# Optimization experiments

Hardware: AMD Instinct MI355X
Metric: run time of the kernel (lower is better)

Reference implementation:

```python
import jax, jax.numpy as jnp
import numpy as np

SCORE_THR = 0.3
NMS_IOU = 0.3
TOPK = 100          # fixed candidate budget replacing dynamic boolean masking
IMAGE_SHAPE = (512, 512)  # (H, W); letterbox_image=False so scale is direct


def pool_nms(heat):
    # 3x3 max-pool peak-NMS: keep only local maxima
    pooled = jax.lax.reduce_window(heat, -jnp.inf, jax.lax.max,
                                   (1, 1, 3, 3), (1, 1, 1, 1), 'SAME')
    return heat * (pooled == heat).astype(heat.dtype)


def setup_inputs() -> dict:
    key = jax.random.key(0)
    k1, k2, k3 = jax.random.split(key, 3)
    hm = jax.random.uniform(k1, (32, 80, 128, 128), dtype=jnp.float32)
    wh = jax.random.uniform(k2, (32, 2, 128, 128), dtype=jnp.float32) * 8.0
    offset = jax.random.uniform(k3, (32, 2, 128, 128), dtype=jnp.float32)
    return {"hm": hm, "wh": wh, "offset": offset}


def reference(hm, wh, offset):
    B, C, H, W = hm.shape
    HW = H * W
    heat = pool_nms(hm)
    heat = heat.transpose(0, 2, 3, 1).reshape(B, HW, C)       # [B,HW,C]
    whf = wh.transpose(0, 2, 3, 1).reshape(B, HW, 2)           # [B,HW,2]
    off = offset.transpose(0, 2, 3, 1).reshape(B, HW, 2)       # [B,HW,2]

    conf = heat.max(-1)                                        # [B,HW]
    cls = jnp.argmax(heat, -1)                                 # [B,HW]

    idx = jnp.arange(HW)
    xv = (idx % W).astype(hm.dtype)
    yv = (idx // W).astype(hm.dtype)
    cx = xv[None, :] + off[..., 0]
    cy = yv[None, :] + off[..., 1]
    bw = whf[..., 0]
    bh = whf[..., 1]
    # normalized xyxy boxes, as in decode_bbox
    boxes = jnp.stack([(cx - bw / 2) / W, (cy - bh / 2) / H,
                       (cx + bw / 2) / W, (cy + bh / 2) / H], -1)  # [B,HW,4]

    scores = jnp.where(conf > SCORE_THR, conf, 0.0)
    top_s, top_i = jax.lax.top_k(scores, TOPK)                 # sorted desc
    tb = jnp.take_along_axis(boxes, top_i[..., None], axis=1)  # [B,K,4]
    tc = jnp.take_along_axis(cls, top_i, axis=1)               # [B,K]
    valid = top_s > SCORE_THR                                  # [B,K]

    # per-class greedy NMS on score-sorted candidates (fixed size K)
    area = (tb[..., 2] - tb[..., 0]) * (tb[..., 3] - tb[..., 1])
    lt = jnp.maximum(tb[:, :, None, :2], tb[:, None, :, :2])
    rb = jnp.minimum(tb[:, :, None, 2:], tb[:, None, :, 2:])
    whi = jnp.clip(rb - lt, 0.0)
    inter = whi[..., 0] * whi[..., 1]
    iou = inter / (area[:, :, None] + area[:, None, :] - inter + 1e-9)
    supmat = (iou > NMS_IOU) & (tc[:, :, None] == tc[:, None, :])  # [B,K,K]

    j = jnp.arange(TOPK)

    def body(i, keep):
        alive_i = jnp.take(keep, i, axis=1)[:, None]           # [B,1]
        sup = jnp.take(supmat, i, axis=1) & (j[None, :] > i) & alive_i
        return keep & ~sup

    keep = jax.lax.fori_loop(0, TOPK, body, valid)             # [B,K]

    # centernet_correct_boxes with letterbox_image=False: scale to image size
    ih, iw = IMAGE_SHAPE
    cxy = (tb[..., :2] + tb[..., 2:]) / 2
    cwh = tb[..., 2:] - tb[..., :2]
    mins = cxy - cwh / 2
    maxs = cxy + cwh / 2
    scale = jnp.array([iw, ih, iw, ih], hm.dtype)
    bimg = jnp.concatenate([mins, maxs], -1) * scale           # [B,K,4]

    dets = jnp.concatenate([bimg, top_s[..., None],
                            tc[..., None].astype(hm.dtype)], -1)  # [B,K,6]
    return jnp.where(keep[..., None], dets, 0.0)
```

## Files before the change

kernel.cpp:

```cpp
#include <hip/hip_runtime.h>
#include <hip/hip_bf16.h>
#include <stdint.h>

#define HH 128
#define WW 128
#define CC 80
#define HW (HH * WW)
#define BB 32
#define TOPK 100
#define TROWS 8
#define NTHREADS 256
#define SCORE_THR 0.3f
#define NMS_IOU 0.3f
#define BUF 512
#define MINT 0x3E99999Bu

__device__ __forceinline__ void async_load16(const float* gp, const float* lp) {
    auto g = (const __attribute__((address_space(1))) void*)(uintptr_t)gp;
    auto l = (__attribute__((address_space(3))) void*)(uint32_t)(uintptr_t)lp;
    __builtin_amdgcn_global_load_lds(g, l, 16, 0, 0);
}

template <int G>
__global__ __launch_bounds__(NTHREADS, 8)
void heat_reduce(const float* __restrict__ hm,
                 float* __restrict__ conf_out,
                 unsigned char* __restrict__ cls_out) {
    constexpr int CPG = CC / G;
    const int g      = blockIdx.x % G;
    const int stripe = (blockIdx.x / G) & 15;
    const int b      = blockIdx.x / (16 * G);
    const int y0     = stripe * TROWS;
    const int tid    = threadIdx.x;
    const int lane   = tid & 63;
    const int wv     = tid >> 6;
    const int x      = tid & 127;
    const int h      = tid >> 7;
    const int c0     = g * CPG;

    __shared__ float tileS[2][(TROWS + 2) * WW];

    auto load = [&](int c, int buf) {
        const float* base = hm + (size_t)(b * CC + c) * HW;
        for (int chunk = wv; chunk < 5; chunk += 4) {
            int e    = chunk * 64 + lane;
            int row  = e >> 5;
            int col  = (e & 31) << 2;
            int y    = y0 - 1 + row;
            y = min(max(y, 0), HH - 1);
            async_load16(base + (size_t)y * WW + col,
                         &tileS[buf][chunk * 256]);
        }
    };

    float conf[4] = {0.f, 0.f, 0.f, 0.f};
    int   cls[4]  = {c0, c0, c0, c0};

    const int xl = (x > 0) ? x - 1 : x;
    const int xr = (x < WW - 1) ? x + 1 : x;

    load(c0, 0);
    __syncthreads();

    for (int cc = 0; cc < CPG; ++cc) {
        const int c  = c0 + cc;
        const int bb = cc & 1;
        if (cc + 1 < CPG) load(c + 1, bb ^ 1);

        float rmax[6], center[6];
#pragma unroll
        for (int k = 0; k < 6; ++k) {
            const float* row = &tileS[bb][(h * 4 + k) * WW];
            float l = row[xl], m = row[x], r = row[xr];
            center[k] = m;
            rmax[k]   = fmaxf(fmaxf(l, m), r);
        }
#pragma unroll
        for (int r = 0; r < 4; ++r) {
            float val  = center[r + 1];
            float pool = fmaxf(fmaxf(rmax[r], rmax[r + 1]), rmax[r + 2]);
            float heat = (val == pool) ? val : 0.0f;
            if (heat > conf[r]) { conf[r] = heat; cls[r] = c; }
        }
        __syncthreads();
    }

#pragma unroll
    for (int r = 0; r < 4; ++r) {
        int y = y0 + h * 4 + r;
        size_t idx = (size_t)b * HW + (size_t)y * WW + x;
        conf_out[idx * G + g] = conf[r];
        cls_out[idx * G + g]  = (unsigned char)cls[r];
    }
}

template <int G>
__global__ __launch_bounds__(NTHREADS, 1)
void select_nms(const float* __restrict__ conf_part,
                const unsigned char* __restrict__ cls_part,
                const float* __restrict__ wh,
                const float* __restrict__ offset,
                float* __restrict__ out) {
    const int b    = blockIdx.x;
    const int tid  = threadIdx.x;
    const int lane = tid & 63;
    const int wid  = tid >> 6;
    constexpr int VALS = HW / NTHREADS;

    __shared__ int wsum[4];
    __shared__ unsigned int sCnt;
    __shared__ unsigned long long keys[BUF];

    unsigned u[VALS];
#pragma unroll
    for (int k = 0; k < VALS; ++k) {
        int i = k * NTHREADS + tid;
        float best;
        if constexpr (G == 4) {
            float4 cf = *(const float4*)&conf_part[(size_t)(b * HW + i) * 4];
            best = cf.x;
            if (cf.y > best) best = cf.y;
            if (cf.z > best) best = cf.z;
            if (cf.w > best) best = cf.w;
        } else {
            best = conf_part[(size_t)b * HW + i];
        }
        u[k] = (best > SCORE_THR) ? __float_as_uint(best) : 0u;
    }

    auto blockCount = [&](unsigned T) -> int {
        int c = 0;
#pragma unroll
        for (int k = 0; k < VALS; ++k) c += (u[k] >= T);
        for (int o = 32; o > 0; o >>= 1) c += __shfl_down(c, o, 64);
        if (lane == 0) wsum[wid] = c;
        __syncthreads();
        int tot = wsum[0] + wsum[1] + wsum[2] + wsum[3];
        __syncthreads();
        return tot;
    };

    unsigned V;
    {
        unsigned lo = MINT, hi = 0x3F800001u;
        int cl = blockCount(lo);
        if (cl < TOPK) {
            V = lo;
        } else {
            while (hi - lo > 1u) {
                unsigned mid = lo + ((hi - lo) >> 1);
                if (blockCount(mid) >= TOPK) lo = mid; else hi = mid;
            }
            V = lo;
        }
    }

    if (tid == 0) sCnt = 0;
    for (int i = tid; i < BUF; i += NTHREADS) keys[i] = 0ull;
    __syncthreads();
#pragma unroll
    for (int k = 0; k < VALS; ++k) {
        if (u[k] >= V) {
            int i = k * NTHREADS + tid;
            unsigned pos = atomicAdd(&sCnt, 1u);
            if (pos < BUF)
                keys[pos] = ((unsigned long long)u[k] << 32) |
                            (unsigned)(HW - 1 - i);
        }
    }
    __syncthreads();
    int cnt = (int)sCnt;
    if (cnt > BUF) cnt = BUF;

    int n = 1;
    while (n < cnt) n <<= 1;
    for (int k = 2; k <= n; k <<= 1) {
        for (int j = k >> 1; j > 0; j >>= 1) {
            for (int i = tid; i < n; i += NTHREADS) {
                int p = i ^ j;
                if (p > i) {
                    unsigned long long a = keys[i], bb2 = keys[p];
                    bool asc_seg = ((i & k) != 0);
                    bool sw = asc_seg ? (a > bb2) : (a < bb2);
                    if (sw) { keys[i] = bb2; keys[p] = a; }
                }
            }
            __syncthreads();
        }
    }

    __shared__ float bx[TOPK][4];
    __shared__ float barea[TOPK];
    __shared__ float bsc[TOPK];
    __shared__ int   bcls[TOPK];
    __shared__ int   keep[TOPK];

    if (tid < TOPK) {
        unsigned long long kk = keys[tid];
        float sc = __uint_as_float((unsigned)(kk >> 32));
        int   i  = HW - 1 - (int)(kk & 0xFFFFFFFFull);
        int   y  = (i >> 7) & 127;
        int   x  = i & 127;
        const float*         cp = conf_part + (size_t)(b * HW + i) * G;
        const unsigned char* kp = cls_part  + (size_t)(b * HW + i) * G;
        float bcf = cp[0]; int bc = kp[0];
#pragma unroll
        for (int gg = 1; gg < G; ++gg)
            if (cp[gg] > bcf) { bcf = cp[gg]; bc = kp[gg]; }

        size_t base = (size_t)b * 2 * HW + (size_t)y * WW + x;
        float ox = offset[base];
        float oy = offset[base + HW];
        float w  = wh[base];
        float hh = wh[base + HW];
        float cx = (float)x + ox;
        float cy = (float)y + oy;
        float x1 = (cx - w  * 0.5f) * (1.0f / 128.0f);
        float y1 = (cy - hh * 0.5f) * (1.0f / 128.0f);
        float x2 = (cx + w  * 0.5f) * (1.0f / 128.0f);
        float y2 = (cy + hh * 0.5f) * (1.0f / 128.0f);
        bx[tid][0] = x1; bx[tid][1] = y1; bx[tid][2] = x2; bx[tid][3] = y2;
        barea[tid] = (x2 - x1) * (y2 - y1);
        bsc[tid]   = sc;
        bcls[tid]  = bc;
        keep[tid]  = (sc > SCORE_THR) ? 1 : 0;
    }
    __syncthreads();

    if (tid < 64) {
        const int A  = tid;
        const int Bq = tid + 64;
        float aX0 = bx[A][0], aY0 = bx[A][1], aX1 = bx[A][2], aY1 = bx[A][3];
        float aAr = barea[A]; int aC = bcls[A]; int kA = keep[A];
        float bX0 = 0, bY0 = 0, bX1 = 0, bY1 = 0, bAr = 0;
        int   bC = -1, kB = 0;
        if (Bq < TOPK) {
            bX0 = bx[Bq][0]; bY0 = bx[Bq][1]; bX1 = bx[Bq][2]; bY1 = bx[Bq][3];
            bAr = barea[Bq]; bC = bcls[Bq]; kB = keep[Bq];
        }
        for (int i = 0; i < TOPK; ++i) {
            int kv    = (i < 64) ? kA : kB;
            int alive = __shfl(kv, i & 63, 64);
            if (alive) {
                float iX0 = bx[i][0], iY0 = bx[i][1];
                float iX1 = bx[i][2], iY1 = bx[i][3];
                float iAr = barea[i]; int iC = bcls[i];
                if (A > i && aC == iC) {
                    float lx = fmaxf(aX0, iX0), ly = fmaxf(aY0, iY0);
                    float rx = fminf(aX1, iX1), ry = fminf(aY1, iY1);
                    float iw = fmaxf(rx - lx, 0.f), ih = fmaxf(ry - ly, 0.f);
                    float inter = iw * ih;
                    float iou = inter / (aAr + iAr - inter + 1e-9f);
                    if (iou > NMS_IOU) kA = 0;
                }
                if (Bq > i && Bq < TOPK && bC == iC) {
                    float lx = fmaxf(bX0, iX0), ly = fmaxf(bY0, iY0);
                    float rx = fminf(bX1, iX1), ry = fminf(bY1, iY1);
                    float iw = fmaxf(rx - lx, 0.f), ih = fmaxf(ry - ly, 0.f);
                    float inter = iw * ih;
                    float iou = inter / (bAr + iAr - inter + 1e-9f);
                    if (iou > NMS_IOU) kB = 0;
                }
            }
        }
        keep[A] = kA;
        if (Bq < TOPK) keep[Bq] = kB;
    }
    __syncthreads();

    for (int t = tid; t < TOPK * 6; t += NTHREADS) {
        int j = t / 6, comp = t - j * 6;
        float v = 0.0f;
        if (keep[j]) {
            if (comp < 4)       v = bx[j][comp] * 512.0f;
            else if (comp == 4) v = bsc[j];
            else                v = (float)bcls[j];
        }
        out[(size_t)b * (TOPK * 6) + t] = v;
    }
}

extern "C" void kernel_launch(void* const* d_in, const int* in_sizes, int n_in,
                              void* d_out, int out_size, void* d_ws, size_t ws_size,
                              hipStream_t stream) {
    const float* hm     = (const float*)d_in[0];
    const float* wh     = (const float*)d_in[1];
    const float* offset = (const float*)d_in[2];
    float* out = (float*)d_out;

    const size_t need4 = (size_t)BB * HW * (4 * 4 + 4);
    if (ws_size >= need4) {
        float* confp = (float*)d_ws;
        unsigned char* clsp = (unsigned char*)d_ws + (size_t)BB * HW * 4 * 4;
        heat_reduce<4><<<BB * 16 * 4, NTHREADS, 0, stream>>>(hm, confp, clsp);
        select_nms<4><<<BB, NTHREADS, 0, stream>>>(confp, clsp, wh, offset, out);
    } else {
        float* confp = (float*)d_ws;
        unsigned char* clsp = (unsigned char*)d_ws + (size_t)BB * HW * 4;
        heat_reduce<1><<<BB * 16 * 1, NTHREADS, 0, stream>>>(hm, confp, clsp);
        select_nms<1><<<BB, NTHREADS, 0, stream>>>(confp, clsp, wh, offset, out);
    }
}
```

Measured before the change: 300.0 us.

## Replace LDS-tiled heatmap pooling with register float4 loads and lane shuffles

```diff
diff --git a/kernel.cpp b/kernel.cpp
--- a/kernel.cpp
+++ b/kernel.cpp
@@ -8,96 +8,77 @@
 #define HW (HH * WW)
 #define BB 32
 #define TOPK 100
-#define TROWS 8
 #define NTHREADS 256
 #define SCORE_THR 0.3f
 #define NMS_IOU 0.3f
 #define BUF 512
 #define MINT 0x3E99999Bu
 
-__device__ __forceinline__ void async_load16(const float* gp, const float* lp) {
-    auto g = (const __attribute__((address_space(1))) void*)(uintptr_t)gp;
-    auto l = (__attribute__((address_space(3))) void*)(uint32_t)(uintptr_t)lp;
-    __builtin_amdgcn_global_load_lds(g, l, 16, 0, 0);
-}
-
-template <int G>
-__global__ __launch_bounds__(NTHREADS, 8)
+__global__ __launch_bounds__(NTHREADS, 2)
 void heat_reduce(const float* __restrict__ hm,
                  float* __restrict__ conf_out,
                  unsigned char* __restrict__ cls_out) {
-    constexpr int CPG = CC / G;
-    const int g      = blockIdx.x % G;
-    const int stripe = (blockIdx.x / G) & 15;
-    const int b      = blockIdx.x / (16 * G);
-    const int y0     = stripe * TROWS;
+    const int stripe = blockIdx.x & 15;
+    const int b      = blockIdx.x >> 4;
     const int tid    = threadIdx.x;
-    const int lane   = tid & 63;
-    const int wv     = tid >> 6;
-    const int x      = tid & 127;
-    const int h      = tid >> 7;
-    const int c0     = g * CPG;
-
-    __shared__ float tileS[2][(TROWS + 2) * WW];
-
-    auto load = [&](int c, int buf) {
-        const float* base = hm + (size_t)(b * CC + c) * HW;
-        for (int chunk = wv; chunk < 5; chunk += 4) {
-            int e    = chunk * 64 + lane;
-            int row  = e >> 5;
-            int col  = (e & 31) << 2;
-            int y    = y0 - 1 + row;
-            y = min(max(y, 0), HH - 1);
-            async_load16(base + (size_t)y * WW + col,
-                         &tileS[buf][chunk * 256]);
-        }
+    const int c31    = tid & 31;
+    const int r      = tid >> 5;
+    const int x4     = c31 << 2;
+    const int y      = stripe * 8 + r;
+    const int yM     = (y > 0) ? y - 1 : 0;
+    const int yP     = (y < HH - 1) ? y + 1 : y;
+    const bool leftClamp  = (c31 == 0);
+    const bool rightClamp = (c31 == 31);
+
+    const float* bbase = hm + (size_t)b * CC * HW;
+    const size_t o0 = (size_t)yM * WW + x4;
+    const size_t o1 = (size_t)y  * WW + x4;
+    const size_t o2 = (size_t)yP * WW + x4;
+
+    float conf[4] = {0.f, 0.f, 0.f, 0.f};
+    int   cls[4]  = {0, 0, 0, 0};
+
+    auto rowmax = [&](float4 a, float rm[4]) {
+        float le = __shfl_up(a.w, 1, 64);
+        float re = __shfl_down(a.x, 1, 64);
+        if (leftClamp)  le = a.x;
+        if (rightClamp) re = a.w;
+        rm[0] = fmaxf(fmaxf(le,  a.x), a.y);
+        rm[1] = fmaxf(fmaxf(a.x, a.y), a.z);
+        rm[2] = fmaxf(fmaxf(a.y, a.z), a.w);
+        rm[3] = fmaxf(fmaxf(a.z, a.w), re);
     };
 
-    float conf[4] = {0.f, 0.f, 0.f, 0.f};
-    int   cls[4]  = {c0, c0, c0, c0};
-
-    const int xl = (x > 0) ? x - 1 : x;
-    const int xr = (x < WW - 1) ? x + 1 : x;
-
-    load(c0, 0);
-    __syncthreads();
-
-    for (int cc = 0; cc < CPG; ++cc) {
-        const int c  = c0 + cc;
-        const int bb = cc & 1;
-        if (cc + 1 < CPG) load(c + 1, bb ^ 1);
-
-        float rmax[6], center[6];
-#pragma unroll
-        for (int k = 0; k < 6; ++k) {
-            const float* row = &tileS[bb][(h * 4 + k) * WW];
-            float l = row[xl], m = row[x], r = row[xr];
-            center[k] = m;
-            rmax[k]   = fmaxf(fmaxf(l, m), r);
-        }
-#pragma unroll
-        for (int r = 0; r < 4; ++r) {
-            float val  = center[r + 1];
-            float pool = fmaxf(fmaxf(rmax[r], rmax[r + 1]), rmax[r + 2]);
-            float heat = (val == pool) ? val : 0.0f;
-            if (heat > conf[r]) { conf[r] = heat; cls[r] = c; }
-        }
-        __syncthreads();
-    }
-
-#pragma unroll
-    for (int r = 0; r < 4; ++r) {
-        int y = y0 + h * 4 + r;
-        size_t idx = (size_t)b * HW + (size_t)y * WW + x;
-        conf_out[idx * G + g] = conf[r];
-        cls_out[idx * G + g]  = (unsigned char)cls[r];
-    }
+#pragma unroll 8
+    for (int c = 0; c < CC; ++c) {
+        const float* p = bbase + (size_t)c * HW;
+        float4 a0 = *(const float4*)(p + o0);
+        float4 a1 = *(const float4*)(p + o1);
+        float4 a2 = *(const float4*)(p + o2);
+        float rm0[4], rm1[4], rm2[4];
+        rowmax(a0, rm0);
+        rowmax(a1, rm1);
+        rowmax(a2, rm2);
+        float ctr[4] = {a1.x, a1.y, a1.z, a1.w};
+#pragma unroll
+        for (int i = 0; i < 4; ++i) {
+            float pool = fmaxf(fmaxf(rm0[i], rm1[i]), rm2[i]);
+            float heat = (ctr[i] == pool) ? ctr[i] : 0.0f;
+            if (heat > conf[i]) { conf[i] = heat; cls[i] = c; }
+        }
+    }
+
+    size_t idx = (size_t)b * HW + (size_t)y * WW + x4;
+    *(float4*)&conf_out[idx] =
+        make_float4(conf[0], conf[1], conf[2], conf[3]);
+    uchar4 cv = make_uchar4((unsigned char)cls[0], (unsigned char)cls[1],
+                            (unsigned char)cls[2], (unsigned char)cls[3]);
+    *(uchar4*)&cls_out[idx] = cv;
 }
 
-template <int G>
 __global__ __launch_bounds__(NTHREADS, 1)
-void select_nms(const float* __restrict__ conf_part,
-                const unsigned char* __restrict__ cls_part,
+void select_nms(const float* __restrict__ conf_m,
+                const unsigned char* __restrict__ cls_m,
                 const float* __restrict__ wh,
                 const float* __restrict__ offset,
                 float* __restrict__ out) {
@@ -115,16 +96,7 @@
 #pragma unroll
     for (int k = 0; k < VALS; ++k) {
         int i = k * NTHREADS + tid;
-        float best;
-        if constexpr (G == 4) {
-            float4 cf = *(const float4*)&conf_part[(size_t)(b * HW + i) * 4];
-            best = cf.x;
-            if (cf.y > best) best = cf.y;
-            if (cf.z > best) best = cf.z;
-            if (cf.w > best) best = cf.w;
-        } else {
-            best = conf_part[(size_t)b * HW + i];
-        }
+        float best = conf_m[(size_t)b * HW + i];
         u[k] = (best > SCORE_THR) ? __float_as_uint(best) : 0u;
     }
 
@@ -201,12 +173,7 @@
         int   i  = HW - 1 - (int)(kk & 0xFFFFFFFFull);
         int   y  = (i >> 7) & 127;
         int   x  = i & 127;
-        const float*         cp = conf_part + (size_t)(b * HW + i) * G;
-        const unsigned char* kp = cls_part  + (size_t)(b * HW + i) * G;
-        float bcf = cp[0]; int bc = kp[0];
-#pragma unroll
-        for (int gg = 1; gg < G; ++gg)
-            if (cp[gg] > bcf) { bcf = cp[gg]; bc = kp[gg]; }
+        int   bc = (int)cls_m[(size_t)b * HW + i];
 
         size_t base = (size_t)b * 2 * HW + (size_t)y * WW + x;
         float ox = offset[base];
@@ -288,16 +255,9 @@
     const float* offset = (const float*)d_in[2];
     float* out = (float*)d_out;
 
-    const size_t need4 = (size_t)BB * HW * (4 * 4 + 4);
-    if (ws_size >= need4) {
-        float* confp = (float*)d_ws;
-        unsigned char* clsp = (unsigned char*)d_ws + (size_t)BB * HW * 4 * 4;
-        heat_reduce<4><<<BB * 16 * 4, NTHREADS, 0, stream>>>(hm, confp, clsp);
-        select_nms<4><<<BB, NTHREADS, 0, stream>>>(confp, clsp, wh, offset, out);
-    } else {
-        float* confp = (float*)d_ws;
-        unsigned char* clsp = (unsigned char*)d_ws + (size_t)BB * HW * 4;
-        heat_reduce<1><<<BB * 16 * 1, NTHREADS, 0, stream>>>(hm, confp, clsp);
-        select_nms<1><<<BB, NTHREADS, 0, stream>>>(confp, clsp, wh, offset, out);
-    }
+    float* confm = (float*)d_ws;
+    unsigned char* clsm = (unsigned char*)d_ws + (size_t)BB * HW * 4;
+
+    heat_reduce<<<BB * 16, NTHREADS, 0, stream>>>(hm, confm, clsm);
+    select_nms<<<BB, NTHREADS, 0, stream>>>(confm, clsm, wh, offset, out);
 }
```

Result: slower. 326.6 us (+8.9%).
